# Optimization experiments

Measured on AMD Instinct MI355X. Metric: run time of the kernel, lower is better.

Reference implementation:

```python
import jax, jax.numpy as jnp
from jax import lax
import numpy as np

IN_DIM = 5
HID = 512
SEQ = 250
BATCH = 256


def setup_inputs() -> dict:
    key = jax.random.key(0)
    ks = jax.random.split(key, 7)
    s = 1.0 / np.sqrt(HID)  # PyTorch LSTMCell init scale
    strokes = jax.random.normal(ks[0], (BATCH, SEQ, IN_DIM), dtype=jnp.float32)
    W_ih = jax.random.uniform(ks[1], (4 * HID, IN_DIM), minval=-s, maxval=s, dtype=jnp.float32)
    W_hh = jax.random.uniform(ks[2], (4 * HID, HID), minval=-s, maxval=s, dtype=jnp.float32)
    b_ih = jax.random.uniform(ks[3], (4 * HID,), minval=-s, maxval=s, dtype=jnp.float32)
    b_hh = jax.random.uniform(ks[4], (4 * HID,), minval=-s, maxval=s, dtype=jnp.float32)
    W_out = jax.random.uniform(ks[5], (1, HID), minval=-s, maxval=s, dtype=jnp.float32)
    b_out = jax.random.uniform(ks[6], (1,), minval=-s, maxval=s, dtype=jnp.float32)
    return {"strokes": strokes, "W_ih": W_ih, "W_hh": W_hh, "b_ih": b_ih,
            "b_hh": b_hh, "W_out": W_out, "b_out": b_out}


def reference(strokes, W_ih, W_hh, b_ih, b_hh, W_out, b_out):
    B = strokes.shape[0]
    # Precompute input projections for all timesteps (one big GEMM instead of SEQ small ones)
    # x_proj: [T, B, 4H]
    x_proj = jnp.einsum('bti,gi->tbg', strokes, W_ih) + b_ih + b_hh
    h0 = jnp.zeros((B, HID), dtype=strokes.dtype)
    c0 = jnp.zeros((B, HID), dtype=strokes.dtype)

    def step(carry, xp):
        h, c = carry
        gates = xp + h @ W_hh.T  # [B, 4H]; PyTorch gate order: i, f, g, o
        i, f, g, o = jnp.split(gates, 4, axis=-1)
        c = jax.nn.sigmoid(f) * c + jax.nn.sigmoid(i) * jnp.tanh(g)
        h = jax.nn.sigmoid(o) * jnp.tanh(c)
        return (h, c), None

    (h, _), _ = lax.scan(step, (h0, c0), x_proj)
    raw = (h @ W_out.T + b_out).squeeze(-1)  # [B]
    return jax.nn.sigmoid(jax.nn.leaky_relu(raw, 0.1))
```

## Files before the change

### kernel.cpp

```cpp
#include <hip/hip_runtime.h>
#include <hip/hip_bf16.h>

#define BATCH 256
#define SEQ   250
#define HID   512
#define INDIM 5

#define NBLK  256
#define NCH   16
#define MB    16
#define HB    32
#define NMEM  16

#define LROWU 36
#define LMEMU 576
#define SLOT_BYTES (BATCH * HID * 2)

typedef __attribute__((ext_vector_type(8))) short short8;
typedef __attribute__((ext_vector_type(4))) float f32x4;
typedef __attribute__((ext_vector_type(4))) unsigned int u32x4;

__device__ __forceinline__ float sigmoidf_fast(float x) {
  return 1.0f / (1.0f + __expf(-x));
}
__device__ __forceinline__ float tanhf_fast(float x) {
  return 2.0f / (1.0f + __expf(-2.0f * x)) - 1.0f;
}
__device__ __forceinline__ unsigned short f2bf_rne(float x) {
  union { float f; unsigned u; } v; v.f = x;
  unsigned r = v.u + 0x7fffu + ((v.u >> 16) & 1u);
  return (unsigned short)(r >> 16);
}
__device__ __forceinline__ float bf2f(unsigned short h) {
  union { unsigned u; float f; } v; v.u = ((unsigned)h) << 16;
  return v.f;
}

__global__ __launch_bounds__(256, 1) void lstm_persist(
    const float* __restrict__ strokes, const float* __restrict__ W_ih,
    const float* __restrict__ W_hh, const float* __restrict__ b_ih,
    const float* __restrict__ b_hh, const float* __restrict__ W_out,
    const float* __restrict__ b_out, float* __restrict__ out,
    unsigned short* __restrict__ hbuf,
    int* __restrict__ flagsML,
    int* __restrict__ flagsL2,
    int* __restrict__ xcd_ids,
    int* __restrict__ vflag)
{
  const int tid  = threadIdx.x;
  const int bid  = blockIdx.x;
  const int bt   = bid & 15;
  const int ht   = bid >> 4;
  const int wv   = tid >> 6;
  const int lane = tid & 63;
  const int n16  = lane & 15;
  const int q    = lane >> 4;

  __shared__ unsigned short h_lds[NMEM * LMEMU];
  __shared__ float g_lds[4][MB][33];
  __shared__ float wih_lds[4][HB][INDIM];
  __shared__ float bias_lds[4][HB];
  __shared__ int fast_s;

  unsigned xcc;
  asm volatile("s_getreg_b32 %0, hwreg(HW_REG_XCC_ID)" : "=s"(xcc));
  xcc &= 0xfu;
  if (tid == 0) {
    __hip_atomic_store(&xcd_ids[bid], (int)xcc, __ATOMIC_RELAXED,
                       __HIP_MEMORY_SCOPE_AGENT);
  }
  if (bid < 16 && wv == 0) {
    int other = (int)xcc;
    if (lane < NMEM) {
      const int* xp = &xcd_ids[bid + 16 * lane];
      other = -1;
      for (int it = 0; it < 16384 && other < 0; ++it) {
        other = __hip_atomic_load(xp, __ATOMIC_RELAXED, __HIP_MEMORY_SCOPE_AGENT);
      }
    }
    unsigned long long ok = __ballot(other == (int)xcc);
    if (lane == 0) {
      __hip_atomic_store(&vflag[bid * 16], (ok == ~0ull) ? 2 : 1,
                         __ATOMIC_RELAXED, __HIP_MEMORY_SCOPE_AGENT);
    }
  }
  if (tid == 0) {
    int v;
    do {
      v = __hip_atomic_load(&vflag[bt * 16], __ATOMIC_RELAXED,
                            __HIP_MEMORY_SCOPE_AGENT);
    } while (v <= 0);
    fast_s = (v == 2) ? 1 : 0;
  }

  if (tid < 128) {
    int g = tid >> 5, j = tid & 31;
    int r = g * HID + ht * HB + j;
    #pragma unroll
    for (int i = 0; i < INDIM; ++i) wih_lds[g][j][i] = W_ih[r * INDIM + i];
    bias_lds[g][j] = b_ih[r] + b_hh[r];
  }

  short8 wfrag[16][2];
  {
    #pragma unroll
    for (int i = 0; i < 16; ++i) {
      const int kb = (wv * 4 + i) & 15;
      #pragma unroll
      for (int nt = 0; nt < 2; ++nt) {
        const float* p = W_hh
            + (size_t)(wv * HID + ht * HB + nt * 16 + n16) * HID
            + kb * 32 + q * 8;
        short8 f;
        #pragma unroll
        for (int j = 0; j < 8; ++j) f[j] = (short)f2bf_rne(p[j]);
        wfrag[i][nt] = f;
      }
    }
  }
  __syncthreads();
  const bool fast = fast_s != 0;

  const int am  = tid >> 4;
  const int ajp = (tid & 15) * 2;
  const int ab  = bt * MB + am;
  const int j0m = wv * 4;
  float c0 = 0.f, c1 = 0.f;

  for (int t = 0; t < SEQ; ++t) {
    unsigned short* hprev = hbuf + (((t & 1) ^ 1) ? (SLOT_BYTES / 2) : 0);
    unsigned short* hcur  = hbuf + ((t & 1) ? (SLOT_BYTES / 2) : 0);

    const float* sp = strokes + ((size_t)ab * SEQ + t) * INDIM;
    float s0 = sp[0], s1 = sp[1], s2 = sp[2], s3 = sp[3], s4 = sp[4];

    f32x4 acc[2][2] = {};
    if (t > 0) {
      if (lane < 16) {
        const int fi = (bt * 16 + (j0m + (lane >> 2))) * 16 + (lane & 3) * 4;
        const int* fpL = &flagsL2[fi];
        const int* fpM = &flagsML[fi];
        if (fast) {
          int v;
          do {
            int v1, v2;
            asm volatile("global_load_dword %0, %2, off sc0\n\t"
                         "global_load_dword %1, %3, off sc0 sc1\n\t"
                         "s_waitcnt vmcnt(0)"
                         : "=v"(v1), "=v"(v2)
                         : "v"(fpL), "v"(fpM)
                         : "memory");
            v = v1 > v2 ? v1 : v2;
          } while (v < t);
        } else {
          while (__hip_atomic_load(fpM, __ATOMIC_RELAXED,
                                   __HIP_MEMORY_SCOPE_AGENT) < t) { }
        }
      }
      const char* base = reinterpret_cast<const char*>(hprev) + bt * 16384
                       + j0m * 1024;
      u32x4 tmp[4];
      if (fast) {
        #pragma unroll
        for (int i = 0; i < 4; ++i)
          asm volatile("global_load_dwordx4 %0, %1, off sc0"
                       : "=v"(tmp[i])
                       : "v"(base + (size_t)(i * 64 + lane) * 16) : "memory");
      } else {
        #pragma unroll
        for (int i = 0; i < 4; ++i)
          asm volatile("global_load_dwordx4 %0, %1, off sc0 sc1"
                       : "=v"(tmp[i])
                       : "v"(base + (size_t)(i * 64 + lane) * 16) : "memory");
      }
      asm volatile("s_waitcnt vmcnt(0)" ::: "memory");
      #pragma unroll
      for (int i = 0; i < 4; ++i) {
        const int idx = i * 64 + lane;
        const int m   = j0m + (idx >> 6);
        const int c   = idx & 63;
        *reinterpret_cast<u32x4*>(
            &h_lds[m * LMEMU + (c >> 2) * LROWU + (c & 3) * 8]) = tmp[i];
      }

      #pragma unroll
      for (int i = 0; i < 4; ++i) {
        const int kb = wv * 4 + i;
        const short8 a = *reinterpret_cast<const short8*>(
            &h_lds[kb * LMEMU + n16 * LROWU + q * 8]);
        #pragma unroll
        for (int nt = 0; nt < 2; ++nt)
          acc[nt][i & 1] = __builtin_amdgcn_mfma_f32_16x16x32_bf16(
              a, wfrag[i][nt], acc[nt][i & 1], 0, 0, 0);
      }
      __syncthreads();
      #pragma unroll
      for (int i = 4; i < 16; ++i) {
        const int kb = (wv * 4 + i) & 15;
        const short8 a = *reinterpret_cast<const short8*>(
            &h_lds[kb * LMEMU + n16 * LROWU + q * 8]);
        #pragma unroll
        for (int nt = 0; nt < 2; ++nt)
          acc[nt][i & 1] = __builtin_amdgcn_mfma_f32_16x16x32_bf16(
              a, wfrag[i][nt], acc[nt][i & 1], 0, 0, 0);
      }
    }

    #pragma unroll
    for (int nt = 0; nt < 2; ++nt) {
      #pragma unroll
      for (int r = 0; r < 4; ++r) {
        g_lds[wv][q * 4 + r][nt * 16 + n16] = acc[nt][0][r] + acc[nt][1][r];
      }
    }
    __syncthreads();

    float hv[2];
    #pragma unroll
    for (int e = 0; e < 2; ++e) {
      const int j = ajp + e;
      float pre[4];
      #pragma unroll
      for (int g = 0; g < 4; ++g) {
        pre[g] = bias_lds[g][j] + g_lds[g][am][j]
               + s0 * wih_lds[g][j][0] + s1 * wih_lds[g][j][1]
               + s2 * wih_lds[g][j][2] + s3 * wih_lds[g][j][3]
               + s4 * wih_lds[g][j][4];
      }
      float ig = sigmoidf_fast(pre[0]);
      float fg = sigmoidf_fast(pre[1]);
      float gg = tanhf_fast(pre[2]);
      float og = sigmoidf_fast(pre[3]);
      float& c = e ? c1 : c0;
      c = fg * c + ig * gg;
      hv[e] = og * tanhf_fast(c);
    }
    unsigned pack = (unsigned)f2bf_rne(hv[0]) | ((unsigned)f2bf_rne(hv[1]) << 16);
    unsigned* hp = reinterpret_cast<unsigned*>(
        reinterpret_cast<char*>(hcur) + bt * 16384 + ht * 1024 + am * 64 + ajp * 2);
    if (fast) {
      asm volatile("global_store_dword %0, %1, off sc0"
                   :: "v"(hp), "v"(pack) : "memory");
    } else {
      __hip_atomic_store(hp, pack, __ATOMIC_RELAXED, __HIP_MEMORY_SCOPE_AGENT);
    }

    asm volatile("s_waitcnt vmcnt(0)" ::: "memory");
    const int gen = t + 1;
    if (lane == 0) {
      const int fi = (bt * 16 + ht) * 16 + wv * 4;
      if (fast) {
        asm volatile("global_store_dword %0, %1, off sc0"
                     :: "v"(&flagsL2[fi]), "v"(gen) : "memory");
      }
      __hip_atomic_store(&flagsML[fi], gen, __ATOMIC_RELAXED,
                         __HIP_MEMORY_SCOPE_AGENT);
    }
  }

  if (ht == 0) {
    if (lane < 16) {
      const int fi = (bt * 16 + (j0m + (lane >> 2))) * 16 + (lane & 3) * 4;
      const int* fpL = &flagsL2[fi];
      const int* fpM = &flagsML[fi];
      if (fast) {
        int v;
        do {
          int v1, v2;
          asm volatile("global_load_dword %0, %2, off sc0\n\t"
                       "global_load_dword %1, %3, off sc0 sc1\n\t"
                       "s_waitcnt vmcnt(0)"
                       : "=v"(v1), "=v"(v2)
                       : "v"(fpL), "v"(fpM)
                       : "memory");
          v = v1 > v2 ? v1 : v2;
        } while (v < SEQ);
      } else {
        while (__hip_atomic_load(fpM, __ATOMIC_RELAXED,
                                 __HIP_MEMORY_SCOPE_AGENT) < SEQ) { }
      }
    }
    const char* base = reinterpret_cast<const char*>(hbuf)
                     + ((SEQ - 1) & 1) * SLOT_BYTES + bt * 16384 + j0m * 1024;
    u32x4 tmp[4];
    if (fast) {
      #pragma unroll
      for (int i = 0; i < 4; ++i)
        asm volatile("global_load_dwordx4 %0, %1, off sc0"
                     : "=v"(tmp[i])
                     : "v"(base + (size_t)(i * 64 + lane) * 16) : "memory");
    } else {
      #pragma unroll
      for (int i = 0; i < 4; ++i)
        asm volatile("global_load_dwordx4 %0, %1, off sc0 sc1"
                     : "=v"(tmp[i])
                     : "v"(base + (size_t)(i * 64 + lane) * 16) : "memory");
    }
    asm volatile("s_waitcnt vmcnt(0)" ::: "memory");
    #pragma unroll
    for (int i = 0; i < 4; ++i) {
      const int idx = i * 64 + lane;
      const int m   = j0m + (idx >> 6);
      const int c   = idx & 63;
      *reinterpret_cast<u32x4*>(
          &h_lds[m * LMEMU + (c >> 2) * LROWU + (c & 3) * 8]) = tmp[i];
    }
    __syncthreads();
    if (tid < MB) {
      const int b = bt * MB + tid;
      float s = 0.f;
      for (int k = 0; k < HID; ++k) {
        s += bf2f(h_lds[(k >> 5) * LMEMU + tid * LROWU + (k & 31)]) * W_out[k];
      }
      float raw = s + b_out[0];
      float lr = raw > 0.f ? raw : 0.1f * raw;
      out[b] = 1.0f / (1.0f + __expf(-lr));
    }
  }
}

extern "C" void kernel_launch(void* const* d_in, const int* in_sizes, int n_in,
                              void* d_out, int out_size, void* d_ws, size_t ws_size,
                              hipStream_t stream) {
  const float* strokes = (const float*)d_in[0];
  const float* W_ih    = (const float*)d_in[1];
  const float* W_hh    = (const float*)d_in[2];
  const float* b_ih    = (const float*)d_in[3];
  const float* b_hh    = (const float*)d_in[4];
  const float* W_out   = (const float*)d_in[5];
  const float* b_out   = (const float*)d_in[6];
  float* out = (float*)d_out;

  char* ws = (char*)d_ws;
  unsigned short* hbuf = (unsigned short*)ws;
  size_t off = (size_t)2 * SLOT_BYTES;
  int* flagsML = (int*)(ws + off);  off += 16384;
  int* flagsL2 = (int*)(ws + off);  off += 16384;
  int* xcd_ids = (int*)(ws + off);  off += 2048;
  int* vflag   = (int*)(ws + off);

  lstm_persist<<<NBLK, 256, 0, stream>>>(strokes, W_ih, W_hh, b_ih, b_hh,
                                         W_out, b_out, out, hbuf,
                                         flagsML, flagsL2, xcd_ids, vflag);
}
```

Before: 842.0 us.

## Remove LDS staging and block barriers; load h fragments directly into MFMA registers

Each wave now loads its h A-fragments straight from global memory into registers and overlaps the loads with MFMAs using staged waitcnts, so the LDS staging buffer and the per-step __syncthreads are gone. The gate columns are interleaved so each wave owns all four gates for its 8 columns. Gate combination is then done with cross-lane shuffles instead of an LDS round trip. Flags are compacted to one per wave and polled with a single dwordx4 load, and the final output dot product uses a shuffle reduction. The cost is more global loads per wave (16 per step instead of 4 shared via LDS), plus more register pressure from holding 16 A fragments.

```diff
diff --git a/kernel.cpp b/kernel.cpp
--- a/kernel.cpp
+++ b/kernel.cpp
@@ -1,5 +1,4 @@
 #include <hip/hip_runtime.h>
-#include <hip/hip_bf16.h>
 
 #define BATCH 256
 #define SEQ   250
@@ -7,18 +6,11 @@
 #define INDIM 5
 
 #define NBLK  256
-#define NCH   16
-#define MB    16
-#define HB    32
-#define NMEM  16
-
-#define LROWU 36
-#define LMEMU 576
 #define SLOT_BYTES (BATCH * HID * 2)
 
 typedef __attribute__((ext_vector_type(8))) short short8;
 typedef __attribute__((ext_vector_type(4))) float f32x4;
-typedef __attribute__((ext_vector_type(4))) unsigned int u32x4;
+typedef __attribute__((ext_vector_type(4))) int   i32x4;
 
 __device__ __forceinline__ float sigmoidf_fast(float x) {
   return 1.0f / (1.0f + __expf(-x));
@@ -55,11 +47,10 @@
   const int lane = tid & 63;
   const int n16  = lane & 15;
   const int q    = lane >> 4;
-
-  __shared__ unsigned short h_lds[NMEM * LMEMU];
-  __shared__ float g_lds[4][MB][33];
-  __shared__ float wih_lds[4][HB][INDIM];
-  __shared__ float bias_lds[4][HB];
+  const int j7   = n16 & 7;
+  const int hi   = n16 >> 3;
+  const int mycol = ht * 32 + wv * 8 + j7;
+
   __shared__ int fast_s;
 
   unsigned xcc;
@@ -71,7 +62,7 @@
   }
   if (bid < 16 && wv == 0) {
     int other = (int)xcc;
-    if (lane < NMEM) {
+    if (lane < 16) {
       const int* xp = &xcd_ids[bid + 16 * lane];
       other = -1;
       for (int it = 0; it < 16384 && other < 0; ++it) {
@@ -93,12 +84,13 @@
     fast_s = (v == 2) ? 1 : 0;
   }
 
-  if (tid < 128) {
-    int g = tid >> 5, j = tid & 31;
-    int r = g * HID + ht * HB + j;
-    #pragma unroll
-    for (int i = 0; i < INDIM; ++i) wih_lds[g][j][i] = W_ih[r * INDIM + i];
-    bias_lds[g][j] = b_ih[r] + b_hh[r];
+  float wih[4][INDIM], bias[4];
+  #pragma unroll
+  for (int g = 0; g < 4; ++g) {
+    const int r = g * HID + mycol;
+    #pragma unroll
+    for (int i = 0; i < INDIM; ++i) wih[g][i] = W_ih[r * INDIM + i];
+    bias[g] = b_ih[r] + b_hh[r];
   }
 
   short8 wfrag[16][2];
@@ -108,9 +100,9 @@
       const int kb = (wv * 4 + i) & 15;
       #pragma unroll
       for (int nt = 0; nt < 2; ++nt) {
-        const float* p = W_hh
-            + (size_t)(wv * HID + ht * HB + nt * 16 + n16) * HID
-            + kb * 32 + q * 8;
+        const int s = nt * 16 + n16;
+        const int row = (s >> 3) * HID + ht * 32 + wv * 8 + (s & 7);
+        const float* p = W_hh + (size_t)row * HID + kb * 32 + q * 8;
         short8 f;
         #pragma unroll
         for (int j = 0; j < 8; ++j) f[j] = (short)f2bf_rne(p[j]);
@@ -121,134 +113,169 @@
   __syncthreads();
   const bool fast = fast_s != 0;
 
-  const int am  = tid >> 4;
-  const int ajp = (tid & 15) * 2;
-  const int ab  = bt * MB + am;
-  const int j0m = wv * 4;
+  const int row0 = q * 4 + 2 * hi;
+  const float* sp0 = strokes + (size_t)(bt * 16 + row0) * SEQ * INDIM;
+  const float* sp1 = sp0 + (size_t)SEQ * INDIM;
+
   float c0 = 0.f, c1 = 0.f;
 
   for (int t = 0; t < SEQ; ++t) {
-    unsigned short* hprev = hbuf + (((t & 1) ^ 1) ? (SLOT_BYTES / 2) : 0);
-    unsigned short* hcur  = hbuf + ((t & 1) ? (SLOT_BYTES / 2) : 0);
-
-    const float* sp = strokes + ((size_t)ab * SEQ + t) * INDIM;
-    float s0 = sp[0], s1 = sp[1], s2 = sp[2], s3 = sp[3], s4 = sp[4];
+    const char* hprev = (const char*)hbuf + (((t & 1) ^ 1) ? SLOT_BYTES : 0);
+    char*       hcur  = (char*)hbuf + ((t & 1) ? SLOT_BYTES : 0);
+
+    float sA[INDIM], sB[INDIM];
+    #pragma unroll
+    for (int i = 0; i < INDIM; ++i) {
+      sA[i] = sp0[t * INDIM + i];
+      sB[i] = sp1[t * INDIM + i];
+    }
 
     f32x4 acc[2][2] = {};
     if (t > 0) {
       if (lane < 16) {
-        const int fi = (bt * 16 + (j0m + (lane >> 2))) * 16 + (lane & 3) * 4;
-        const int* fpL = &flagsL2[fi];
-        const int* fpM = &flagsML[fi];
+        const int* fpL = &flagsL2[(bt * 16 + lane) * 4];
+        const int* fpM = &flagsML[(bt * 16 + lane) * 4];
         if (fast) {
-          int v;
+          int m;
           do {
-            int v1, v2;
-            asm volatile("global_load_dword %0, %2, off sc0\n\t"
-                         "global_load_dword %1, %3, off sc0 sc1\n\t"
+            i32x4 vL, vM;
+            asm volatile("global_load_dwordx4 %0, %2, off sc0\n\t"
+                         "global_load_dwordx4 %1, %3, off sc0 sc1\n\t"
                          "s_waitcnt vmcnt(0)"
-                         : "=v"(v1), "=v"(v2)
-                         : "v"(fpL), "v"(fpM)
-                         : "memory");
-            v = v1 > v2 ? v1 : v2;
-          } while (v < t);
+                         : "=v"(vL), "=v"(vM)
+                         : "v"(fpL), "v"(fpM) : "memory");
+            int a0 = vL[0] > vM[0] ? vL[0] : vM[0];
+            int a1 = vL[1] > vM[1] ? vL[1] : vM[1];
+            int a2 = vL[2] > vM[2] ? vL[2] : vM[2];
+            int a3 = vL[3] > vM[3] ? vL[3] : vM[3];
+            int m0 = a0 < a1 ? a0 : a1;
+            int m1 = a2 < a3 ? a2 : a3;
+            m = m0 < m1 ? m0 : m1;
+          } while (m < t);
         } else {
-          while (__hip_atomic_load(fpM, __ATOMIC_RELAXED,
-                                   __HIP_MEMORY_SCOPE_AGENT) < t) { }
+          int m;
+          do {
+            i32x4 v;
+            asm volatile("global_load_dwordx4 %0, %1, off sc0 sc1\n\t"
+                         "s_waitcnt vmcnt(0)"
+                         : "=v"(v) : "v"(fpM) : "memory");
+            int m0 = v[0] < v[1] ? v[0] : v[1];
+            int m1 = v[2] < v[3] ? v[2] : v[3];
+            m = m0 < m1 ? m0 : m1;
+          } while (m < t);
         }
       }
-      const char* base = reinterpret_cast<const char*>(hprev) + bt * 16384
-                       + j0m * 1024;
-      u32x4 tmp[4];
+      short8 afrag[16];
+      const char* ab = hprev + bt * 16384 + n16 * 64 + q * 16;
       if (fast) {
         #pragma unroll
-        for (int i = 0; i < 4; ++i)
+        for (int i = 0; i < 16; ++i) {
+          const int kb = (wv * 4 + i) & 15;
           asm volatile("global_load_dwordx4 %0, %1, off sc0"
-                       : "=v"(tmp[i])
-                       : "v"(base + (size_t)(i * 64 + lane) * 16) : "memory");
+                       : "=v"(afrag[i]) : "v"(ab + kb * 1024) : "memory");
+        }
       } else {
         #pragma unroll
-        for (int i = 0; i < 4; ++i)
+        for (int i = 0; i < 16; ++i) {
+          const int kb = (wv * 4 + i) & 15;
           asm volatile("global_load_dwordx4 %0, %1, off sc0 sc1"
-                       : "=v"(tmp[i])
-                       : "v"(base + (size_t)(i * 64 + lane) * 16) : "memory");
+                       : "=v"(afrag[i]) : "v"(ab + kb * 1024) : "memory");
+        }
+      }
+      asm volatile("s_waitcnt vmcnt(12)" ::: "memory");
+      __builtin_amdgcn_sched_barrier(0);
+      #pragma unroll
+      for (int i = 0; i < 4; ++i) {
+        acc[0][i & 1] = __builtin_amdgcn_mfma_f32_16x16x32_bf16(
+            afrag[i], wfrag[i][0], acc[0][i & 1], 0, 0, 0);
+        acc[1][i & 1] = __builtin_amdgcn_mfma_f32_16x16x32_bf16(
+            afrag[i], wfrag[i][1], acc[1][i & 1], 0, 0, 0);
+      }
+      asm volatile("s_waitcnt vmcnt(8)" ::: "memory");
+      __builtin_amdgcn_sched_barrier(0);
+      #pragma unroll
+      for (int i = 4; i < 8; ++i) {
+        acc[0][i & 1] = __builtin_amdgcn_mfma_f32_16x16x32_bf16(
+            afrag[i], wfrag[i][0], acc[0][i & 1], 0, 0, 0);
+        acc[1][i & 1] = __builtin_amdgcn_mfma_f32_16x16x32_bf16(
+            afrag[i], wfrag[i][1], acc[1][i & 1], 0, 0, 0);
+      }
+      asm volatile("s_waitcnt vmcnt(4)" ::: "memory");
+      __builtin_amdgcn_sched_barrier(0);
+      #pragma unroll
+      for (int i = 8; i < 12; ++i) {
+        acc[0][i & 1] = __builtin_amdgcn_mfma_f32_16x16x32_bf16(
+            afrag[i], wfrag[i][0], acc[0][i & 1], 0, 0, 0);
+        acc[1][i & 1] = __builtin_amdgcn_mfma_f32_16x16x32_bf16(
+            afrag[i], wfrag[i][1], acc[1][i & 1], 0, 0, 0);
       }
       asm volatile("s_waitcnt vmcnt(0)" ::: "memory");
-      #pragma unroll
-      for (int i = 0; i < 4; ++i) {
-        const int idx = i * 64 + lane;
-        const int m   = j0m + (idx >> 6);
-        const int c   = idx & 63;
-        *reinterpret_cast<u32x4*>(
-            &h_lds[m * LMEMU + (c >> 2) * LROWU + (c & 3) * 8]) = tmp[i];
-      }
-
-      #pragma unroll
-      for (int i = 0; i < 4; ++i) {
-        const int kb = wv * 4 + i;
-        const short8 a = *reinterpret_cast<const short8*>(
-            &h_lds[kb * LMEMU + n16 * LROWU + q * 8]);
-        #pragma unroll
-        for (int nt = 0; nt < 2; ++nt)
-          acc[nt][i & 1] = __builtin_amdgcn_mfma_f32_16x16x32_bf16(
-              a, wfrag[i][nt], acc[nt][i & 1], 0, 0, 0);
-      }
-      __syncthreads();
-      #pragma unroll
-      for (int i = 4; i < 16; ++i) {
-        const int kb = (wv * 4 + i) & 15;
-        const short8 a = *reinterpret_cast<const short8*>(
-            &h_lds[kb * LMEMU + n16 * LROWU + q * 8]);
-        #pragma unroll
-        for (int nt = 0; nt < 2; ++nt)
-          acc[nt][i & 1] = __builtin_amdgcn_mfma_f32_16x16x32_bf16(
-              a, wfrag[i][nt], acc[nt][i & 1], 0, 0, 0);
-      }
-    }
-
-    #pragma unroll
-    for (int nt = 0; nt < 2; ++nt) {
-      #pragma unroll
-      for (int r = 0; r < 4; ++r) {
-        g_lds[wv][q * 4 + r][nt * 16 + n16] = acc[nt][0][r] + acc[nt][1][r];
-      }
-    }
-    __syncthreads();
-
-    float hv[2];
+      __builtin_amdgcn_sched_barrier(0);
+      #pragma unroll
+      for (int i = 12; i < 16; ++i) {
+        acc[0][i & 1] = __builtin_amdgcn_mfma_f32_16x16x32_bf16(
+            afrag[i], wfrag[i][0], acc[0][i & 1], 0, 0, 0);
+        acc[1][i & 1] = __builtin_amdgcn_mfma_f32_16x16x32_bf16(
+            afrag[i], wfrag[i][1], acc[1][i & 1], 0, 0, 0);
+      }
+    }
+
+    const f32x4 S0 = acc[0][0] + acc[0][1];
+    const f32x4 S1 = acc[1][0] + acc[1][1];
+    float hv0 = 0.f, hv1 = 0.f;
     #pragma unroll
     for (int e = 0; e < 2; ++e) {
-      const int j = ajp + e;
-      float pre[4];
-      #pragma unroll
-      for (int g = 0; g < 4; ++g) {
-        pre[g] = bias_lds[g][j] + g_lds[g][am][j]
-               + s0 * wih_lds[g][j][0] + s1 * wih_lds[g][j][1]
-               + s2 * wih_lds[g][j][2] + s3 * wih_lds[g][j][3]
-               + s4 * wih_lds[g][j][4];
-      }
-      float ig = sigmoidf_fast(pre[0]);
-      float fg = sigmoidf_fast(pre[1]);
-      float gg = tanhf_fast(pre[2]);
-      float og = sigmoidf_fast(pre[3]);
+      float mine0 = hi ? S0[2 + e] : S0[e];
+      float send0 = hi ? S0[e]     : S0[2 + e];
+      float mine1 = hi ? S1[2 + e] : S1[e];
+      float send1 = hi ? S1[e]     : S1[2 + e];
+      float got0 = __shfl_xor(send0, 8);
+      float got1 = __shfl_xor(send1, 8);
+      float pi = hi ? got0  : mine0;
+      float pf = hi ? mine0 : got0;
+      float pg = hi ? got1  : mine1;
+      float po = hi ? mine1 : got1;
+      const float* s = e ? sB : sA;
+      pi += bias[0] + s[0]*wih[0][0] + s[1]*wih[0][1] + s[2]*wih[0][2]
+                    + s[3]*wih[0][3] + s[4]*wih[0][4];
+      pf += bias[1] + s[0]*wih[1][0] + s[1]*wih[1][1] + s[2]*wih[1][2]
+                    + s[3]*wih[1][3] + s[4]*wih[1][4];
+      pg += bias[2] + s[0]*wih[2][0] + s[1]*wih[2][1] + s[2]*wih[2][2]
+                    + s[3]*wih[2][3] + s[4]*wih[2][4];
+      po += bias[3] + s[0]*wih[3][0] + s[1]*wih[3][1] + s[2]*wih[3][2]
+                    + s[3]*wih[3][3] + s[4]*wih[3][4];
+      float ig = sigmoidf_fast(pi);
+      float fg = sigmoidf_fast(pf);
+      float gg = tanhf_fast(pg);
+      float og = sigmoidf_fast(po);
       float& c = e ? c1 : c0;
       c = fg * c + ig * gg;
-      hv[e] = og * tanhf_fast(c);
-    }
-    unsigned pack = (unsigned)f2bf_rne(hv[0]) | ((unsigned)f2bf_rne(hv[1]) << 16);
-    unsigned* hp = reinterpret_cast<unsigned*>(
-        reinterpret_cast<char*>(hcur) + bt * 16384 + ht * 1024 + am * 64 + ajp * 2);
-    if (fast) {
-      asm volatile("global_store_dword %0, %1, off sc0"
-                   :: "v"(hp), "v"(pack) : "memory");
-    } else {
-      __hip_atomic_store(hp, pack, __ATOMIC_RELAXED, __HIP_MEMORY_SCOPE_AGENT);
+      float hv = og * tanhf_fast(c);
+      if (e == 0) hv0 = hv; else hv1 = hv;
+    }
+
+    {
+      float sendh = (j7 & 1) ? hv0 : hv1;
+      float rh = __shfl_xor(sendh, 1);
+      unsigned lo = (j7 & 1) ? (unsigned)f2bf_rne(rh)  : (unsigned)f2bf_rne(hv0);
+      unsigned hh = (j7 & 1) ? (unsigned)f2bf_rne(hv1) : (unsigned)f2bf_rne(rh);
+      unsigned pack = lo | (hh << 16);
+      const int srow = row0 + (j7 & 1);
+      const int colp = wv * 8 + (j7 & ~1);
+      unsigned* hp = reinterpret_cast<unsigned*>(
+          hcur + bt * 16384 + ht * 1024 + srow * 64 + colp * 2);
+      if (fast) {
+        asm volatile("global_store_dword %0, %1, off sc0"
+                     :: "v"(hp), "v"(pack) : "memory");
+      } else {
+        __hip_atomic_store(hp, pack, __ATOMIC_RELAXED, __HIP_MEMORY_SCOPE_AGENT);
+      }
     }
 
     asm volatile("s_waitcnt vmcnt(0)" ::: "memory");
     const int gen = t + 1;
     if (lane == 0) {
-      const int fi = (bt * 16 + ht) * 16 + wv * 4;
+      const int fi = (bt * 16 + ht) * 4 + wv;
       if (fast) {
         asm volatile("global_store_dword %0, %1, off sc0"
                      :: "v"(&flagsL2[fi]), "v"(gen) : "memory");
@@ -260,61 +287,68 @@
 
   if (ht == 0) {
     if (lane < 16) {
-      const int fi = (bt * 16 + (j0m + (lane >> 2))) * 16 + (lane & 3) * 4;
-      const int* fpL = &flagsL2[fi];
-      const int* fpM = &flagsML[fi];
+      const int* fpL = &flagsL2[(bt * 16 + lane) * 4];
+      const int* fpM = &flagsML[(bt * 16 + lane) * 4];
       if (fast) {
-        int v;
+        int m;
         do {
-          int v1, v2;
-          asm volatile("global_load_dword %0, %2, off sc0\n\t"
-                       "global_load_dword %1, %3, off sc0 sc1\n\t"
+          i32x4 vL, vM;
+          asm volatile("global_load_dwordx4 %0, %2, off sc0\n\t"
+                       "global_load_dwordx4 %1, %3, off sc0 sc1\n\t"
                        "s_waitcnt vmcnt(0)"
-                       : "=v"(v1), "=v"(v2)
-                       : "v"(fpL), "v"(fpM)
-                       : "memory");
-          v = v1 > v2 ? v1 : v2;
-        } while (v < SEQ);
+                       : "=v"(vL), "=v"(vM)
+                       : "v"(fpL), "v"(fpM) : "memory");
+          int a0 = vL[0] > vM[0] ? vL[0] : vM[0];
+          int a1 = vL[1] > vM[1] ? vL[1] : vM[1];
+          int a2 = vL[2] > vM[2] ? vL[2] : vM[2];
+          int a3 = vL[3] > vM[3] ? vL[3] : vM[3];
+          int m0 = a0 < a1 ? a0 : a1;
+          int m1 = a2 < a3 ? a2 : a3;
+          m = m0 < m1 ? m0 : m1;
+        } while (m < SEQ);
       } else {
-        while (__hip_atomic_load(fpM, __ATOMIC_RELAXED,
-                                 __HIP_MEMORY_SCOPE_AGENT) < SEQ) { }
-      }
-    }
-    const char* base = reinterpret_cast<const char*>(hbuf)
-                     + ((SEQ - 1) & 1) * SLOT_BYTES + bt * 16384 + j0m * 1024;
-    u32x4 tmp[4];
+        int m;
+        do {
+          i32x4 v;
+          asm volatile("global_load_dwordx4 %0, %1, off sc0 sc1\n\t"
+                       "s_waitcnt vmcnt(0)"
+                       : "=v"(v) : "v"(fpM) : "memory");
+          int m0 = v[0] < v[1] ? v[0] : v[1];
+          int m1 = v[2] < v[3] ? v[2] : v[3];
+          m = m0 < m1 ? m0 : m1;
+        } while (m < SEQ);
+      }
+    }
+    const int frow = wv * 4 + q;
+    const char* hb = (const char*)hbuf + ((SEQ - 1) & 1) * SLOT_BYTES
+                   + bt * 16384 + n16 * 1024 + frow * 64;
+    short8 hvv[4];
     if (fast) {
       #pragma unroll
       for (int i = 0; i < 4; ++i)
         asm volatile("global_load_dwordx4 %0, %1, off sc0"
-                     : "=v"(tmp[i])
-                     : "v"(base + (size_t)(i * 64 + lane) * 16) : "memory");
+                     : "=v"(hvv[i]) : "v"(hb + i * 16) : "memory");
     } else {
       #pragma unroll
       for (int i = 0; i < 4; ++i)
         asm volatile("global_load_dwordx4 %0, %1, off sc0 sc1"
-                     : "=v"(tmp[i])
-                     : "v"(base + (size_t)(i * 64 + lane) * 16) : "memory");
+                     : "=v"(hvv[i]) : "v"(hb + i * 16) : "memory");
     }
     asm volatile("s_waitcnt vmcnt(0)" ::: "memory");
-    #pragma unroll
-    for (int i = 0; i < 4; ++i) {
-      const int idx = i * 64 + lane;
-      const int m   = j0m + (idx >> 6);
-      const int c   = idx & 63;
-      *reinterpret_cast<u32x4*>(
-          &h_lds[m * LMEMU + (c >> 2) * LROWU + (c & 3) * 8]) = tmp[i];
-    }
-    __syncthreads();
-    if (tid < MB) {
-      const int b = bt * MB + tid;
-      float s = 0.f;
-      for (int k = 0; k < HID; ++k) {
-        s += bf2f(h_lds[(k >> 5) * LMEMU + tid * LROWU + (k & 31)]) * W_out[k];
-      }
-      float raw = s + b_out[0];
+    float ssum = 0.f;
+    #pragma unroll
+    for (int v = 0; v < 4; ++v) {
+      #pragma unroll
+      for (int j = 0; j < 8; ++j) {
+        ssum += bf2f((unsigned short)hvv[v][j]) * W_out[n16 * 32 + v * 8 + j];
+      }
+    }
+    #pragma unroll
+    for (int d = 1; d < 16; d <<= 1) ssum += __shfl_xor(ssum, d);
+    if (n16 == 0) {
+      float raw = ssum + b_out[0];
       float lr = raw > 0.f ? raw : 0.1f * raw;
-      out[b] = 1.0f / (1.0f + __expf(-lr));
+      out[bt * 16 + frow] = 1.0f / (1.0f + __expf(-lr));
     }
   }
 }
```

Result: slower. 2.074 ms (+146.4%).

## Permute W_hh rows so gate nonlinearity runs in MFMA registers without LDS

Applied to the files above, without the earlier changes.

Reorders the W_hh fragment rows so each wave's MFMA output tile holds all four gates (i,f,g,o) for its own hidden columns. The gate combination then happens in registers using lane shuffles, which removes the g_lds round trip and a per-step __syncthreads. Input weights and biases move from LDS into per-thread registers, and the h output pack uses a shuffle to pair adjacent columns. The cost is higher register pressure and more shuffle traffic on the serial recurrence path.

```diff
diff --git a/kernel.cpp b/kernel.cpp
--- a/kernel.cpp
+++ b/kernel.cpp
@@ -1,5 +1,4 @@
 #include <hip/hip_runtime.h>
-#include <hip/hip_bf16.h>
 
 #define BATCH 256
 #define SEQ   250
@@ -55,11 +54,11 @@
   const int lane = tid & 63;
   const int n16  = lane & 15;
   const int q    = lane >> 4;
+  const int j7   = n16 & 7;
+  const int hi   = n16 >> 3;
+  const int mycol = ht * HB + wv * 8 + j7;
 
   __shared__ unsigned short h_lds[NMEM * LMEMU];
-  __shared__ float g_lds[4][MB][33];
-  __shared__ float wih_lds[4][HB][INDIM];
-  __shared__ float bias_lds[4][HB];
   __shared__ int fast_s;
 
   unsigned xcc;
@@ -93,12 +92,13 @@
     fast_s = (v == 2) ? 1 : 0;
   }
 
-  if (tid < 128) {
-    int g = tid >> 5, j = tid & 31;
-    int r = g * HID + ht * HB + j;
-    #pragma unroll
-    for (int i = 0; i < INDIM; ++i) wih_lds[g][j][i] = W_ih[r * INDIM + i];
-    bias_lds[g][j] = b_ih[r] + b_hh[r];
+  float wih[4][INDIM], bias[4];
+  #pragma unroll
+  for (int g = 0; g < 4; ++g) {
+    const int r = g * HID + mycol;
+    #pragma unroll
+    for (int i = 0; i < INDIM; ++i) wih[g][i] = W_ih[r * INDIM + i];
+    bias[g] = b_ih[r] + b_hh[r];
   }
 
   short8 wfrag[16][2];
@@ -108,9 +108,9 @@
       const int kb = (wv * 4 + i) & 15;
       #pragma unroll
       for (int nt = 0; nt < 2; ++nt) {
-        const float* p = W_hh
-            + (size_t)(wv * HID + ht * HB + nt * 16 + n16) * HID
-            + kb * 32 + q * 8;
+        const int s = nt * 16 + n16;
+        const int row = (s >> 3) * HID + ht * HB + wv * 8 + (s & 7);
+        const float* p = W_hh + (size_t)row * HID + kb * 32 + q * 8;
         short8 f;
         #pragma unroll
         for (int j = 0; j < 8; ++j) f[j] = (short)f2bf_rne(p[j]);
@@ -121,9 +121,10 @@
   __syncthreads();
   const bool fast = fast_s != 0;
 
-  const int am  = tid >> 4;
-  const int ajp = (tid & 15) * 2;
-  const int ab  = bt * MB + am;
+  const int row0 = q * 4 + 2 * hi;
+  const float* sp0 = strokes + (size_t)(bt * MB + row0) * SEQ * INDIM;
+  const float* sp1 = sp0 + (size_t)SEQ * INDIM;
+
   const int j0m = wv * 4;
   float c0 = 0.f, c1 = 0.f;
 
@@ -131,8 +132,12 @@
     unsigned short* hprev = hbuf + (((t & 1) ^ 1) ? (SLOT_BYTES / 2) : 0);
     unsigned short* hcur  = hbuf + ((t & 1) ? (SLOT_BYTES / 2) : 0);
 
-    const float* sp = strokes + ((size_t)ab * SEQ + t) * INDIM;
-    float s0 = sp[0], s1 = sp[1], s2 = sp[2], s3 = sp[3], s4 = sp[4];
+    float sA[INDIM], sB[INDIM];
+    #pragma unroll
+    for (int i = 0; i < INDIM; ++i) {
+      sA[i] = sp0[t * INDIM + i];
+      sB[i] = sp1[t * INDIM + i];
+    }
 
     f32x4 acc[2][2] = {};
     if (t > 0) {
@@ -206,43 +211,57 @@
       }
     }
 
-    #pragma unroll
-    for (int nt = 0; nt < 2; ++nt) {
-      #pragma unroll
-      for (int r = 0; r < 4; ++r) {
-        g_lds[wv][q * 4 + r][nt * 16 + n16] = acc[nt][0][r] + acc[nt][1][r];
-      }
-    }
-    __syncthreads();
-
-    float hv[2];
+    const f32x4 S0 = acc[0][0] + acc[0][1];
+    const f32x4 S1 = acc[1][0] + acc[1][1];
+    float hv0 = 0.f, hv1 = 0.f;
     #pragma unroll
     for (int e = 0; e < 2; ++e) {
-      const int j = ajp + e;
-      float pre[4];
-      #pragma unroll
-      for (int g = 0; g < 4; ++g) {
-        pre[g] = bias_lds[g][j] + g_lds[g][am][j]
-               + s0 * wih_lds[g][j][0] + s1 * wih_lds[g][j][1]
-               + s2 * wih_lds[g][j][2] + s3 * wih_lds[g][j][3]
-               + s4 * wih_lds[g][j][4];
-      }
-      float ig = sigmoidf_fast(pre[0]);
-      float fg = sigmoidf_fast(pre[1]);
-      float gg = tanhf_fast(pre[2]);
-      float og = sigmoidf_fast(pre[3]);
+      float mine0 = hi ? S0[2 + e] : S0[e];
+      float send0 = hi ? S0[e]     : S0[2 + e];
+      float mine1 = hi ? S1[2 + e] : S1[e];
+      float send1 = hi ? S1[e]     : S1[2 + e];
+      float got0 = __shfl_xor(send0, 8);
+      float got1 = __shfl_xor(send1, 8);
+      float pi = hi ? got0  : mine0;
+      float pf = hi ? mine0 : got0;
+      float pg = hi ? got1  : mine1;
+      float po = hi ? mine1 : got1;
+      const float* s = e ? sB : sA;
+      pi += bias[0] + s[0]*wih[0][0] + s[1]*wih[0][1] + s[2]*wih[0][2]
+                    + s[3]*wih[0][3] + s[4]*wih[0][4];
+      pf += bias[1] + s[0]*wih[1][0] + s[1]*wih[1][1] + s[2]*wih[1][2]
+                    + s[3]*wih[1][3] + s[4]*wih[1][4];
+      pg += bias[2] + s[0]*wih[2][0] + s[1]*wih[2][1] + s[2]*wih[2][2]
+                    + s[3]*wih[2][3] + s[4]*wih[2][4];
+      po += bias[3] + s[0]*wih[3][0] + s[1]*wih[3][1] + s[2]*wih[3][2]
+                    + s[3]*wih[3][3] + s[4]*wih[3][4];
+      float ig = sigmoidf_fast(pi);
+      float fg = sigmoidf_fast(pf);
+      float gg = tanhf_fast(pg);
+      float og = sigmoidf_fast(po);
       float& c = e ? c1 : c0;
       c = fg * c + ig * gg;
-      hv[e] = og * tanhf_fast(c);
-    }
-    unsigned pack = (unsigned)f2bf_rne(hv[0]) | ((unsigned)f2bf_rne(hv[1]) << 16);
-    unsigned* hp = reinterpret_cast<unsigned*>(
-        reinterpret_cast<char*>(hcur) + bt * 16384 + ht * 1024 + am * 64 + ajp * 2);
-    if (fast) {
-      asm volatile("global_store_dword %0, %1, off sc0"
-                   :: "v"(hp), "v"(pack) : "memory");
-    } else {
-      __hip_atomic_store(hp, pack, __ATOMIC_RELAXED, __HIP_MEMORY_SCOPE_AGENT);
+      float hv = og * tanhf_fast(c);
+      if (e == 0) hv0 = hv; else hv1 = hv;
+    }
+
+    {
+      float sendh = (j7 & 1) ? hv0 : hv1;
+      float rh = __shfl_xor(sendh, 1);
+      unsigned lo = (j7 & 1) ? (unsigned)f2bf_rne(rh)  : (unsigned)f2bf_rne(hv0);
+      unsigned hh = (j7 & 1) ? (unsigned)f2bf_rne(hv1) : (unsigned)f2bf_rne(rh);
+      unsigned pack = lo | (hh << 16);
+      const int srow = row0 + (j7 & 1);
+      const int colp = wv * 8 + (j7 & ~1);
+      unsigned* hp = reinterpret_cast<unsigned*>(
+          reinterpret_cast<char*>(hcur) + bt * 16384 + ht * 1024
+          + srow * 64 + colp * 2);
+      if (fast) {
+        asm volatile("global_store_dword %0, %1, off sc0"
+                     :: "v"(hp), "v"(pack) : "memory");
+      } else {
+        __hip_atomic_store(hp, pack, __ATOMIC_RELAXED, __HIP_MEMORY_SCOPE_AGENT);
+      }
     }
 
     asm volatile("s_waitcnt vmcnt(0)" ::: "memory");
```

Measured after the change: 866.6 us. +2.9%, slower.
